# Performance work log

Measured on AMD Instinct MI355X. Metric: run time of the kernel, lower is better.

## Reference

```python
import jax, jax.numpy as jnp
import numpy as np

N = 50000        # nodes
E = 800000       # edges (before self-loops)
F_IN = 256       # input feature dim
HID = 64         # hidden per head (concat=False -> head mean)
NCLS = 40        # classes
HEADS = 8
NEG_SLOPE = 0.2  # PyG GATConv default leaky_relu slope


def setup_inputs() -> dict:
    key = jax.random.key(0)
    ks = jax.random.split(key, 11)
    s = 0.1
    return {
        "x": jax.random.normal(ks[0], (N, F_IN), jnp.float32),
        "edge_index": jax.random.randint(ks[1], (2, E), 0, N, dtype=jnp.int64),
        "edge_attr": jax.random.uniform(ks[2], (E, 1), jnp.float32),
        "W0": jax.random.normal(ks[3], (HEADS * HID, F_IN), jnp.float32) * s,
        "a0s": jax.random.normal(ks[4], (HEADS, HID), jnp.float32) * s,
        "a0d": jax.random.normal(ks[5], (HEADS, HID), jnp.float32) * s,
        "b0": jnp.zeros((HID,), jnp.float32),
        "W2": jax.random.normal(ks[6], (HEADS * NCLS, HID), jnp.float32) * s,
        "a2s": jax.random.normal(ks[7], (HEADS, NCLS), jnp.float32) * s,
        "a2d": jax.random.normal(ks[8], (HEADS, NCLS), jnp.float32) * s,
        "b2": jnp.zeros((NCLS,), jnp.float32),
    }


def _gat_conv(x, src, dst, W, att_src, att_dst, bias, heads, out_c):
    # Linear: [N, in] @ [heads*out, in]^T -> [N, heads, out]
    h = (x @ W.T).reshape(N, heads, out_c)
    # Per-node attention logits, gathered per edge.
    a_s = jnp.einsum('nhc,hc->nh', h, att_src)
    a_d = jnp.einsum('nhc,hc->nh', h, att_dst)
    e = jax.nn.leaky_relu(a_s[src] + a_d[dst], NEG_SLOPE)  # [E, H]
    # Segment softmax over incoming edges of each destination node.
    m = jax.ops.segment_max(e, dst, num_segments=N)
    p = jnp.exp(e - m[dst])
    denom = jax.ops.segment_sum(p, dst, num_segments=N)
    alpha = p / (denom[dst] + 1e-16)
    # Weighted message scatter-sum: [E,H,C] -> [N,H,C]
    out = jax.ops.segment_sum(alpha[:, :, None] * h[src], dst, num_segments=N)
    # concat=False -> mean over heads, then bias.
    return out.mean(axis=1) + bias


def reference(x, edge_index, edge_attr, W0, a0s, a0d, b0, W2, a2s, a2d, b2):
    # edge_attr is unpacked by the torch forward but never used by GATConv.
    # PyG GATConv adds self-loops by default.
    loops = jnp.arange(N, dtype=edge_index.dtype)
    src = jnp.concatenate([edge_index[0], loops])
    dst = jnp.concatenate([edge_index[1], loops])
    h = jax.nn.relu(_gat_conv(x, src, dst, W0, a0s, a0d, b0, HEADS, HID))
    # dropout is identity in eval mode
    out = _gat_conv(h, src, dst, W2, a2s, a2d, b2, HEADS, NCLS)
    return jax.nn.log_softmax(out, axis=1)
```

## Files before the change

### kernel.cpp

```cpp
#include <hip/hip_runtime.h>
#include <hip/hip_bf16.h>
#include <math.h>


#define NEG_SLOPE 0.2f

typedef short v8s __attribute__((ext_vector_type(8)));
typedef float v4f __attribute__((ext_vector_type(4)));
typedef float v2f __attribute__((ext_vector_type(2)));
typedef unsigned short u16;
typedef unsigned int u32;
typedef unsigned char u8;

__device__ __forceinline__ u16 f2bf(float f) {
    union { float f; u32 u; } v; v.f = f;
    u32 r = v.u + 0x7fffu + ((v.u >> 16) & 1u);
    return (u16)(r >> 16);
}
__device__ __forceinline__ float lrelu_exp(float e) {
    e = (e > 0.f) ? e : NEG_SLOPE * e;
    return __expf(e);
}
__device__ __forceinline__ void dec8(uint2 r, float* h) {
    v2f a = __builtin_amdgcn_cvt_pk_f32_fp8(r.x, false);
    v2f b = __builtin_amdgcn_cvt_pk_f32_fp8(r.x, true);
    v2f c = __builtin_amdgcn_cvt_pk_f32_fp8(r.y, false);
    v2f d = __builtin_amdgcn_cvt_pk_f32_fp8(r.y, true);
    h[0] = a.x; h[1] = a.y; h[2] = b.x; h[3] = b.y;
    h[4] = c.x; h[5] = c.y; h[6] = d.x; h[7] = d.y;
}
__device__ __forceinline__ u8 enc8(float v) {
    u32 p = __builtin_amdgcn_cvt_pk_fp8_f32(v, v, 0u, false);
    return (u8)(p & 0xffu);
}


__global__ __launch_bounds__(256) void hist_k(const int* __restrict__ ei, int* __restrict__ deg,
                                              int E, int Nn) {
    int e = blockIdx.x * 256 + threadIdx.x;
    int ET = E + Nn;
    if (e >= ET) return;
    int d = (e < E) ? ei[E + e] : (e - E);
    atomicAdd(&deg[d], 1);
}

__global__ __launch_bounds__(1024) void scanA_k(const int* __restrict__ deg, int* __restrict__ incl,
                                                int* __restrict__ bsum, int n) {
    __shared__ int wsum[16];
    int t = threadIdx.x;
    int i = blockIdx.x * 1024 + t;
    int v = (i < n) ? deg[i] : 0;
    int lane = t & 63, wid = t >> 6;
    int sv = v;
    for (int off = 1; off < 64; off <<= 1) {
        int u = __shfl_up(sv, off, 64);
        if (lane >= off) sv += u;
    }
    if (lane == 63) wsum[wid] = sv;
    __syncthreads();
    if (t < 16) {
        int w = wsum[t];
        for (int off = 1; off < 16; off <<= 1) {
            int u = __shfl_up(w, off, 64);
            if (t >= off) w += u;
        }
        wsum[t] = w;
    }
    __syncthreads();
    int pre = (wid > 0) ? wsum[wid - 1] : 0;
    int inc = pre + sv;
    if (i < n) incl[i] = inc;
    if (t == 1023) bsum[blockIdx.x] = inc;
}

__global__ __launch_bounds__(64) void scanB_k(const int* __restrict__ bsum, int* __restrict__ boff, int B) {
    int t = threadIdx.x;
    int v = (t < B) ? bsum[t] : 0;
    int sv = v;
    for (int off = 1; off < 64; off <<= 1) {
        int u = __shfl_up(sv, off, 64);
        if (t >= off) sv += u;
    }
    if (t < B) boff[t] = sv - v;
    if (t == 63) boff[B] = sv;
}

__global__ __launch_bounds__(256) void scanC_k(const int* __restrict__ incl, const int* __restrict__ deg,
                                               const int* __restrict__ boff, int* __restrict__ rowstart,
                                               int n, int B) {
    int i = blockIdx.x * 256 + threadIdx.x;
    if (i < n) rowstart[i] = boff[i >> 10] + incl[i] - deg[i];
    if (i == 0) rowstart[n] = boff[B];
}

__global__ __launch_bounds__(256) void scatter_k(const int* __restrict__ ei,
                                                 const int* __restrict__ rowstart,
                                                 int* __restrict__ cursor,
                                                 int* __restrict__ srcs, int E, int Nn) {
    int e = blockIdx.x * 256 + threadIdx.x;
    int ET = E + Nn;
    if (e >= ET) return;
    int s, d;
    if (e < E) { s = ei[e]; d = ei[E + e]; }
    else       { s = e - E; d = e - E; }
    int pos = atomicAdd(&cursor[d], 1);
    srcs[rowstart[d] + pos] = s;
}


__global__ __launch_bounds__(256) void cast3_k(const float* __restrict__ x, u16* __restrict__ xb, int nx,
                                               const float* __restrict__ W0, u16* __restrict__ W0b, int n0,
                                               const float* __restrict__ W2, u16* __restrict__ W2b, int n2) {
    int i = (blockIdx.x * 256 + threadIdx.x) * 4;
    const float* in; u16* out;
    if (i < nx)            { in = x;  out = xb; }
    else if (i < nx + n0)  { in = W0; out = W0b; i -= nx; }
    else if (i < nx + n0 + n2) { in = W2; out = W2b; i -= nx + n0; }
    else return;
    float4 v = *reinterpret_cast<const float4*>(in + i);
    ushort4 o;
    o.x = f2bf(v.x); o.y = f2bf(v.y); o.z = f2bf(v.z); o.w = f2bf(v.w);
    *reinterpret_cast<ushort4*>(out + i) = o;
}


__global__ __launch_bounds__(256, 4) void gemm_mfma(const u16* __restrict__ Ab,
                                                    const u16* __restrict__ Bb,
                                                    u8* __restrict__ Cf, int M, int Nc, int K,
                                                    const float* __restrict__ avs_vec,
                                                    const float* __restrict__ avd_vec,
                                                    float* as_out, float* ad_out) {
    __shared__ __align__(16) u8 lds[27648];
    u16 (*As)[72] = reinterpret_cast<u16(*)[72]>(lds);
    u16 (*Bs)[72] = reinterpret_cast<u16(*)[72]>(lds + 18432);
    const int t = threadIdx.x;
    const int m0 = blockIdx.x * 128;
    const int n0 = blockIdx.y * 64;
    const int w = t >> 6, lane = t & 63;
    const int wr = w * 32;
    const int q = lane >> 4, l16 = lane & 15;

    v4f acc[2][4];
#pragma unroll
    for (int i = 0; i < 2; i++)
#pragma unroll
        for (int j = 0; j < 4; j++) acc[i][j] = (v4f){0.f, 0.f, 0.f, 0.f};

    for (int kt = 0; kt < K; kt += 64) {
#pragma unroll
        for (int it = 0; it < 4; it++) {
            int c = it * 256 + t;
            int row = c >> 3, col8 = (c & 7) * 8;
            int gm = m0 + row;
            uint4 va = make_uint4(0u, 0u, 0u, 0u);
            if (gm < M) va = *reinterpret_cast<const uint4*>(Ab + (size_t)gm * K + kt + col8);
            *reinterpret_cast<uint4*>(&As[row][col8]) = va;
        }
#pragma unroll
        for (int it = 0; it < 2; it++) {
            int c = it * 256 + t;
            int row = c >> 3, col8 = (c & 7) * 8;
            uint4 vb = *reinterpret_cast<const uint4*>(Bb + (size_t)(n0 + row) * K + kt + col8);
            *reinterpret_cast<uint4*>(&Bs[row][col8]) = vb;
        }
        __syncthreads();
#pragma unroll
        for (int ks = 0; ks < 2; ks++) {
            v8s af[2], bf[4];
#pragma unroll
            for (int i = 0; i < 2; i++)
                af[i] = *reinterpret_cast<const v8s*>(&As[wr + i * 16 + l16][ks * 32 + q * 8]);
#pragma unroll
            for (int j = 0; j < 4; j++)
                bf[j] = *reinterpret_cast<const v8s*>(&Bs[j * 16 + l16][ks * 32 + q * 8]);
#pragma unroll
            for (int i = 0; i < 2; i++)
#pragma unroll
                for (int j = 0; j < 4; j++)
                    acc[i][j] = __builtin_amdgcn_mfma_f32_16x16x32_bf16(af[i], bf[j], acc[i][j], 0, 0, 0);
        }
        __syncthreads();
    }

    const bool do_att = (as_out != nullptr);
    float avs[4], avd[4];
    if (do_att) {
#pragma unroll
        for (int j = 0; j < 4; j++) {
            avs[j] = avs_vec[n0 + j * 16 + l16];
            avd[j] = avd_vec[n0 + j * 16 + l16];
        }
    }
    const int head = n0 >> 6;

    u8* Cs = lds;
#pragma unroll
    for (int i = 0; i < 2; i++) {
#pragma unroll
        for (int r = 0; r < 4; r++) {
            int row = wr + i * 16 + q * 4 + r;
#pragma unroll
            for (int j = 0; j < 4; j++)
                Cs[row * 80 + j * 16 + l16] = enc8(acc[i][j][r]);
            if (do_att) {
                int gm = m0 + row;
                float ps = 0.f, pd = 0.f;
#pragma unroll
                for (int j = 0; j < 4; j++) {
                    float v = acc[i][j][r];
                    ps = fmaf(v, avs[j], ps);
                    pd = fmaf(v, avd[j], pd);
                }
#pragma unroll
                for (int m = 1; m < 16; m <<= 1) {
                    ps += __shfl_xor(ps, m, 64);
                    pd += __shfl_xor(pd, m, 64);
                }
                if (l16 == 0 && gm < M) {
                    as_out[gm * 8 + head] = ps;
                    ad_out[gm * 8 + head] = pd;
                }
            }
        }
    }
    __syncthreads();
#pragma unroll
    for (int it = 0; it < 2; it++) {
        int idx = it * 256 + t;
        int row = idx >> 2, ch = idx & 3;
        int gm = m0 + row;
        if (gm < M)
            *reinterpret_cast<uint4*>(Cf + (size_t)gm * Nc + n0 + ch * 16) =
                *reinterpret_cast<const uint4*>(&Cs[row * 80 + ch * 16]);
    }
}


__global__ __launch_bounds__(256) void agg1_k(const u8* __restrict__ h1f,
                                              const float* __restrict__ as1, const float* __restrict__ ad1,
                                              const int* __restrict__ srcs, const int* __restrict__ rowstart,
                                              const float* __restrict__ b0, u16* __restrict__ x1b, int Nn) {
    int wave = threadIdx.x >> 6, lane = threadIdx.x & 63;
    int n = blockIdx.x * 4 + wave;
    if (n >= Nn) return;
    const int hl = lane >> 3;
    const float adl = ad1[n * 8 + hl];
    const u32 loff = (u32)lane * 8u;
    float acc[8] = {0, 0, 0, 0, 0, 0, 0, 0};
    float dsum = 0.f;
    int beg = rowstart[n], end = rowstart[n + 1];
    int i = beg;
    for (; i + 8 <= end; i += 8) {
        int s[8];
#pragma unroll
        for (int u = 0; u < 8; u++) s[u] = __builtin_amdgcn_readfirstlane(srcs[i + u]);
        uint2 rw[8];
#pragma unroll
        for (int u = 0; u < 8; u++) rw[u] = *reinterpret_cast<const uint2*>(h1f + ((u32)s[u] * 512u + loff));
        float eg[8];
#pragma unroll
        for (int u = 0; u < 8; u++) eg[u] = as1[(u32)s[u] * 8u + hl];
        float p[8];
#pragma unroll
        for (int u = 0; u < 8; u++) { p[u] = lrelu_exp(eg[u] + adl); dsum += p[u]; }
#pragma unroll
        for (int u = 0; u < 8; u++) {
            float hv[8];
            dec8(rw[u], hv);
#pragma unroll
            for (int j = 0; j < 8; j++) acc[j] = fmaf(p[u], hv[j], acc[j]);
        }
    }
    for (; i < end; i++) {
        int s = __builtin_amdgcn_readfirstlane(srcs[i]);
        uint2 raw = *reinterpret_cast<const uint2*>(h1f + ((u32)s * 512u + loff));
        float p = lrelu_exp(as1[(u32)s * 8u + hl] + adl);
        dsum += p;
        float hv[8];
        dec8(raw, hv);
#pragma unroll
        for (int j = 0; j < 8; j++) acc[j] = fmaf(p, hv[j], acc[j]);
    }
    float inv = 1.f / (dsum + 1e-16f);
    float r[8];
#pragma unroll
    for (int j = 0; j < 8; j++) r[j] = acc[j] * inv;
#pragma unroll
    for (int j = 0; j < 8; j++) {
        r[j] += __shfl_xor(r[j], 8, 64);
        r[j] += __shfl_xor(r[j], 16, 64);
        r[j] += __shfl_xor(r[j], 32, 64);
    }
    if (lane < 8) {
        u16 o[8];
#pragma unroll
        for (int j = 0; j < 8; j++) {
            float v = r[j] * 0.125f + b0[lane * 8 + j];
            o[j] = f2bf((v > 0.f) ? v : 0.f);
        }
        *reinterpret_cast<uint4*>(x1b + (size_t)n * 64 + lane * 8) =
            *reinterpret_cast<const uint4*>(o);
    }
}


__global__ __launch_bounds__(256) void att2_k(const u8* __restrict__ h2f,
                                              const float* __restrict__ a2s, const float* __restrict__ a2d,
                                              float* __restrict__ as2, float* __restrict__ ad2, int Nn) {
    int t = blockIdx.x * 256 + threadIdx.x;
    if (t >= Nn * 8) return;
    int n = t >> 3, h = t & 7;
    const u8* hr = h2f + (size_t)n * 320 + h * 40;
    float s1 = 0.f, s2 = 0.f;
#pragma unroll
    for (int b = 0; b < 5; b++) {
        uint2 raw = *reinterpret_cast<const uint2*>(hr + b * 8);
        float h8[8];
        dec8(raw, h8);
#pragma unroll
        for (int j = 0; j < 8; j++) {
            int c = h * 40 + b * 8 + j;
            s1 = fmaf(h8[j], a2s[c], s1);
            s2 = fmaf(h8[j], a2d[c], s2);
        }
    }
    as2[t] = s1;
    ad2[t] = s2;
}


__global__ __launch_bounds__(256) void agg2_k(const u8* __restrict__ h2f,
                                              const float* __restrict__ as2, const float* __restrict__ ad2,
                                              const int* __restrict__ srcs, const int* __restrict__ rowstart,
                                              const float* __restrict__ b2, float* __restrict__ out, int Nn) {
    __shared__ float smem[4][320];
    int wave = threadIdx.x >> 6, lane = threadIdx.x & 63;
    int n = blockIdx.x * 4 + wave;
    bool active = (n < Nn);
    bool ld = active && (lane < 40);
    const int hl = lane / 5;
    float adl = ld ? ad2[n * 8 + hl] : 0.f;
    float acc[8] = {0, 0, 0, 0, 0, 0, 0, 0};
    float dsum = 0.f;
    if (ld) {
        const u32 loff = (u32)lane * 8u;
        int beg = rowstart[n], end = rowstart[n + 1];
        int i = beg;
        for (; i + 8 <= end; i += 8) {
            int s[8];
#pragma unroll
            for (int u = 0; u < 8; u++) s[u] = __builtin_amdgcn_readfirstlane(srcs[i + u]);
            uint2 rw[8];
#pragma unroll
            for (int u = 0; u < 8; u++) rw[u] = *reinterpret_cast<const uint2*>(h2f + ((u32)s[u] * 320u + loff));
            float eg[8];
#pragma unroll
            for (int u = 0; u < 8; u++) eg[u] = as2[(u32)s[u] * 8u + hl];
            float p[8];
#pragma unroll
            for (int u = 0; u < 8; u++) { p[u] = lrelu_exp(eg[u] + adl); dsum += p[u]; }
#pragma unroll
            for (int u = 0; u < 8; u++) {
                float hv[8];
                dec8(rw[u], hv);
#pragma unroll
                for (int j = 0; j < 8; j++) acc[j] = fmaf(p[u], hv[j], acc[j]);
            }
        }
        for (; i < end; i++) {
            int s = __builtin_amdgcn_readfirstlane(srcs[i]);
            uint2 raw = *reinterpret_cast<const uint2*>(h2f + ((u32)s * 320u + loff));
            float p = lrelu_exp(as2[(u32)s * 8u + hl] + adl);
            dsum += p;
            float hv[8];
            dec8(raw, hv);
#pragma unroll
            for (int j = 0; j < 8; j++) acc[j] = fmaf(p, hv[j], acc[j]);
        }
        float inv = 1.f / (dsum + 1e-16f);
#pragma unroll
        for (int j = 0; j < 8; j++) smem[wave][lane * 8 + j] = acc[j] * inv;
    }
    __syncthreads();
    if (active) {
        float v;
        if (lane < 40) {
            float ssum = 0.f;
#pragma unroll
            for (int h = 0; h < 8; h++) ssum += smem[wave][h * 40 + lane];
            v = ssum * 0.125f + b2[lane];
        } else {
            v = -INFINITY;
        }
        float m = v;
        for (int off = 32; off > 0; off >>= 1) m = fmaxf(m, __shfl_xor(m, off, 64));
        float ex = (lane < 40) ? __expf(v - m) : 0.f;
        float se = ex;
        for (int off = 32; off > 0; off >>= 1) se += __shfl_xor(se, off, 64);
        if (lane < 40) out[(size_t)n * 40 + lane] = v - m - __logf(se);
    }
}


extern "C" void kernel_launch(void* const* d_in, const int* in_sizes, int n_in,
                              void* d_out, int out_size, void* d_ws, size_t ws_size,
                              hipStream_t stream) {
    const float* x   = (const float*)d_in[0];
    const int*   ei  = (const int*)d_in[1];
    const float* W0  = (const float*)d_in[3];
    const float* a0s = (const float*)d_in[4];
    const float* a0d = (const float*)d_in[5];
    const float* b0  = (const float*)d_in[6];
    const float* W2  = (const float*)d_in[7];
    const float* a2s = (const float*)d_in[8];
    const float* a2d = (const float*)d_in[9];
    const float* b2  = (const float*)d_in[10];
    float* out = (float*)d_out;

    const int Nn = in_sizes[0] / 256;
    const int E  = in_sizes[1] / 2;
    const int ET = E + Nn;
    const int NB = (Nn + 1023) / 1024;

    size_t off = 0;
    auto carve = [&](size_t bytes) -> void* {
        void* p = (char*)d_ws + off;
        off += (bytes + 255) & ~(size_t)255;
        return p;
    };
    u16*   xb       = (u16*)carve((size_t)Nn * 256 * 2);
    u16*   W0b      = (u16*)carve((size_t)512 * 256 * 2);
    u16*   W2b      = (u16*)carve((size_t)320 * 64 * 2);
    u8*    h1f      = (u8*)carve((size_t)Nn * 512);
    u16*   x1b      = (u16*)carve((size_t)Nn * 64 * 2);
    u8*    h2f      = (u8*)carve((size_t)Nn * 320);
    float* as1      = (float*)carve((size_t)Nn * 8 * 4);
    float* ad1      = (float*)carve((size_t)Nn * 8 * 4);
    float* as2      = (float*)carve((size_t)Nn * 8 * 4);
    float* ad2      = (float*)carve((size_t)Nn * 8 * 4);
    int*   deg      = (int*)carve((size_t)Nn * 4);
    int*   cursor   = (int*)carve((size_t)Nn * 4);
    int*   rowstart = (int*)carve((size_t)(Nn + 1) * 4);
    int*   srcs     = (int*)carve((size_t)ET * 4);
    int*   incl     = (int*)carve((size_t)Nn * 4);
    int*   bsum     = (int*)carve(64 * 4);
    int*   boff     = (int*)carve(65 * 4);

    const size_t degPad = ((size_t)Nn * 4 + 255) & ~(size_t)255;
    hipMemsetAsync(deg, 0, degPad + (size_t)Nn * 4, stream);

    hist_k<<<(ET + 255) / 256, 256, 0, stream>>>(ei, deg, E, Nn);
    scanA_k<<<NB, 1024, 0, stream>>>(deg, incl, bsum, Nn);
    scanB_k<<<1, 64, 0, stream>>>(bsum, boff, NB);
    scanC_k<<<(Nn + 255) / 256, 256, 0, stream>>>(incl, deg, boff, rowstart, Nn, NB);
    scatter_k<<<(ET + 255) / 256, 256, 0, stream>>>(ei, rowstart, cursor, srcs, E, Nn);

    const int nx = Nn * 256, n0c = 512 * 256, n2c = 320 * 64;
    cast3_k<<<((nx + n0c + n2c) / 4 + 255) / 256, 256, 0, stream>>>(
        x, xb, nx, W0, W0b, n0c, W2, W2b, n2c);

    gemm_mfma<<<dim3((Nn + 127) / 128, 8), 256, 0, stream>>>(
        xb, W0b, h1f, Nn, 512, 256, a0s, a0d, as1, ad1);
    agg1_k<<<(Nn + 3) / 4, 256, 0, stream>>>(h1f, as1, ad1, srcs, rowstart, b0, x1b, Nn);

    gemm_mfma<<<dim3((Nn + 127) / 128, 5), 256, 0, stream>>>(
        x1b, W2b, h2f, Nn, 320, 64, nullptr, nullptr, nullptr, nullptr);
    att2_k<<<(Nn * 8 + 255) / 256, 256, 0, stream>>>(h2f, a2s, a2d, as2, ad2, Nn);
    agg2_k<<<(Nn + 3) / 4, 256, 0, stream>>>(h2f, as2, ad2, srcs, rowstart, b2, out, Nn);
}
```

Before: 399.6 us.

## Fuse CSR build and bf16 casts into one cooperative persistent kernel

Replaces the memset, histogram, three scan kernels, scatter, and cast kernel with a single cooperative kernel using grid-wide syncs between phases. It is meant to remove several kernel launch gaps and the separate memset. The cast work is folded into the first phase alongside the zeroing. The risk is that grid.sync barriers and a fixed grid of 256 blocks of 1024 threads may underuse the GPU for the bandwidth-heavy cast and scatter phases.

```diff
diff --git a/kernel.cpp b/kernel.cpp
--- a/kernel.cpp
+++ b/kernel.cpp
@@ -1,9 +1,12 @@
 #include <hip/hip_runtime.h>
 #include <hip/hip_bf16.h>
+#include <hip/hip_cooperative_groups.h>
 #include <math.h>
 
 
 #define NEG_SLOPE 0.2f
+
+namespace cg = cooperative_groups;
 
 typedef short v8s __attribute__((ext_vector_type(8)));
 typedef float v4f __attribute__((ext_vector_type(4)));
@@ -35,92 +38,93 @@
 }
 
 
-__global__ __launch_bounds__(256) void hist_k(const int* __restrict__ ei, int* __restrict__ deg,
-                                              int E, int Nn) {
-    int e = blockIdx.x * 256 + threadIdx.x;
-    int ET = E + Nn;
-    if (e >= ET) return;
-    int d = (e < E) ? ei[E + e] : (e - E);
-    atomicAdd(&deg[d], 1);
-}
-
-__global__ __launch_bounds__(1024) void scanA_k(const int* __restrict__ deg, int* __restrict__ incl,
-                                                int* __restrict__ bsum, int n) {
+__global__ __launch_bounds__(1024) void prep_k(const float* __restrict__ x, u16* __restrict__ xb,
+                                               const float* __restrict__ W0, u16* __restrict__ W0b,
+                                               const float* __restrict__ W2, u16* __restrict__ W2b,
+                                               int nx, int n0c, int n2c,
+                                               const int* __restrict__ ei, int* __restrict__ deg,
+                                               int* __restrict__ cursor, int* __restrict__ incl,
+                                               int* __restrict__ bsum, int* __restrict__ rowstart,
+                                               int* __restrict__ srcs, int E, int Nn, int NB) {
+    cg::grid_group grid = cg::this_grid();
     __shared__ int wsum[16];
-    int t = threadIdx.x;
-    int i = blockIdx.x * 1024 + t;
-    int v = (i < n) ? deg[i] : 0;
-    int lane = t & 63, wid = t >> 6;
-    int sv = v;
-    for (int off = 1; off < 64; off <<= 1) {
-        int u = __shfl_up(sv, off, 64);
-        if (lane >= off) sv += u;
-    }
-    if (lane == 63) wsum[wid] = sv;
+    __shared__ int sb[65];
+    const int T = gridDim.x * blockDim.x;
+    const int tid = blockIdx.x * blockDim.x + threadIdx.x;
+    const int ET = E + Nn;
+
+    for (int i = tid; i < Nn; i += T) { deg[i] = 0; cursor[i] = 0; }
+    const int tot4 = (nx + n0c + n2c) >> 2;
+    for (int i4 = tid; i4 < tot4; i4 += T) {
+        int i = i4 << 2;
+        const float* in; u16* out;
+        if (i < nx)            { in = x;  out = xb; }
+        else if (i < nx + n0c) { in = W0; out = W0b; i -= nx; }
+        else                   { in = W2; out = W2b; i -= nx + n0c; }
+        float4 v = *reinterpret_cast<const float4*>(in + i);
+        ushort4 o;
+        o.x = f2bf(v.x); o.y = f2bf(v.y); o.z = f2bf(v.z); o.w = f2bf(v.w);
+        *reinterpret_cast<ushort4*>(out + i) = o;
+    }
+    grid.sync();
+
+    for (int e = tid; e < ET; e += T) {
+        int d = (e < E) ? ei[E + e] : (e - E);
+        atomicAdd(&deg[d], 1);
+    }
+    grid.sync();
+
+    if (blockIdx.x < NB) {
+        int t = threadIdx.x;
+        int i = blockIdx.x * 1024 + t;
+        int v = (i < Nn) ? deg[i] : 0;
+        int lane = t & 63, wid = t >> 6;
+        int sv = v;
+        for (int off = 1; off < 64; off <<= 1) {
+            int u = __shfl_up(sv, off, 64);
+            if (lane >= off) sv += u;
+        }
+        if (lane == 63) wsum[wid] = sv;
+        __syncthreads();
+        if (t < 16) {
+            int w = wsum[t];
+            for (int off = 1; off < 16; off <<= 1) {
+                int u = __shfl_up(w, off, 64);
+                if (t >= off) w += u;
+            }
+            wsum[t] = w;
+        }
+        __syncthreads();
+        int pre = (wid > 0) ? wsum[wid - 1] : 0;
+        int inc = pre + sv;
+        if (i < Nn) incl[i] = inc;
+        if (t == 1023) bsum[blockIdx.x] = inc;
+    }
+    grid.sync();
+
+    if (threadIdx.x < 64) {
+        int t = threadIdx.x;
+        int v = (t < NB) ? bsum[t] : 0;
+        int sv = v;
+        for (int off = 1; off < 64; off <<= 1) {
+            int u = __shfl_up(sv, off, 64);
+            if (t >= off) sv += u;
+        }
+        sb[t] = sv - v;
+        if (t == 63) sb[64] = sv;
+    }
     __syncthreads();
-    if (t < 16) {
-        int w = wsum[t];
-        for (int off = 1; off < 16; off <<= 1) {
-            int u = __shfl_up(w, off, 64);
-            if (t >= off) w += u;
-        }
-        wsum[t] = w;
-    }
-    __syncthreads();
-    int pre = (wid > 0) ? wsum[wid - 1] : 0;
-    int inc = pre + sv;
-    if (i < n) incl[i] = inc;
-    if (t == 1023) bsum[blockIdx.x] = inc;
-}
-
-__global__ __launch_bounds__(64) void scanB_k(const int* __restrict__ bsum, int* __restrict__ boff, int B) {
-    int t = threadIdx.x;
-    int v = (t < B) ? bsum[t] : 0;
-    int sv = v;
-    for (int off = 1; off < 64; off <<= 1) {
-        int u = __shfl_up(sv, off, 64);
-        if (t >= off) sv += u;
-    }
-    if (t < B) boff[t] = sv - v;
-    if (t == 63) boff[B] = sv;
-}
-
-__global__ __launch_bounds__(256) void scanC_k(const int* __restrict__ incl, const int* __restrict__ deg,
-                                               const int* __restrict__ boff, int* __restrict__ rowstart,
-                                               int n, int B) {
-    int i = blockIdx.x * 256 + threadIdx.x;
-    if (i < n) rowstart[i] = boff[i >> 10] + incl[i] - deg[i];
-    if (i == 0) rowstart[n] = boff[B];
-}
-
-__global__ __launch_bounds__(256) void scatter_k(const int* __restrict__ ei,
-                                                 const int* __restrict__ rowstart,
-                                                 int* __restrict__ cursor,
-                                                 int* __restrict__ srcs, int E, int Nn) {
-    int e = blockIdx.x * 256 + threadIdx.x;
-    int ET = E + Nn;
-    if (e >= ET) return;
-    int s, d;
-    if (e < E) { s = ei[e]; d = ei[E + e]; }
-    else       { s = e - E; d = e - E; }
-    int pos = atomicAdd(&cursor[d], 1);
-    srcs[rowstart[d] + pos] = s;
-}
-
-
-__global__ __launch_bounds__(256) void cast3_k(const float* __restrict__ x, u16* __restrict__ xb, int nx,
-                                               const float* __restrict__ W0, u16* __restrict__ W0b, int n0,
-                                               const float* __restrict__ W2, u16* __restrict__ W2b, int n2) {
-    int i = (blockIdx.x * 256 + threadIdx.x) * 4;
-    const float* in; u16* out;
-    if (i < nx)            { in = x;  out = xb; }
-    else if (i < nx + n0)  { in = W0; out = W0b; i -= nx; }
-    else if (i < nx + n0 + n2) { in = W2; out = W2b; i -= nx + n0; }
-    else return;
-    float4 v = *reinterpret_cast<const float4*>(in + i);
-    ushort4 o;
-    o.x = f2bf(v.x); o.y = f2bf(v.y); o.z = f2bf(v.z); o.w = f2bf(v.w);
-    *reinterpret_cast<ushort4*>(out + i) = o;
+    for (int i = tid; i < Nn; i += T) rowstart[i] = sb[i >> 10] + incl[i] - deg[i];
+    if (tid == 0) rowstart[Nn] = sb[64];
+    grid.sync();
+
+    for (int e = tid; e < ET; e += T) {
+        int s, d;
+        if (e < E) { s = ei[e]; d = ei[E + e]; }
+        else       { s = e - E; d = e - E; }
+        int pos = atomicAdd(&cursor[d], 1);
+        srcs[rowstart[d] + pos] = s;
+    }
 }
 
 
@@ -417,10 +421,10 @@
     const float* b2  = (const float*)d_in[10];
     float* out = (float*)d_out;
 
-    const int Nn = in_sizes[0] / 256;
-    const int E  = in_sizes[1] / 2;
+    int Nn = in_sizes[0] / 256;
+    int E  = in_sizes[1] / 2;
     const int ET = E + Nn;
-    const int NB = (Nn + 1023) / 1024;
+    int NB = (Nn + 1023) / 1024;
 
     size_t off = 0;
     auto carve = [&](size_t bytes) -> void* {
@@ -444,20 +448,16 @@
     int*   srcs     = (int*)carve((size_t)ET * 4);
     int*   incl     = (int*)carve((size_t)Nn * 4);
     int*   bsum     = (int*)carve(64 * 4);
-    int*   boff     = (int*)carve(65 * 4);
-
-    const size_t degPad = ((size_t)Nn * 4 + 255) & ~(size_t)255;
-    hipMemsetAsync(deg, 0, degPad + (size_t)Nn * 4, stream);
-
-    hist_k<<<(ET + 255) / 256, 256, 0, stream>>>(ei, deg, E, Nn);
-    scanA_k<<<NB, 1024, 0, stream>>>(deg, incl, bsum, Nn);
-    scanB_k<<<1, 64, 0, stream>>>(bsum, boff, NB);
-    scanC_k<<<(Nn + 255) / 256, 256, 0, stream>>>(incl, deg, boff, rowstart, Nn, NB);
-    scatter_k<<<(ET + 255) / 256, 256, 0, stream>>>(ei, rowstart, cursor, srcs, E, Nn);
-
-    const int nx = Nn * 256, n0c = 512 * 256, n2c = 320 * 64;
-    cast3_k<<<((nx + n0c + n2c) / 4 + 255) / 256, 256, 0, stream>>>(
-        x, xb, nx, W0, W0b, n0c, W2, W2b, n2c);
+
+    int nx = Nn * 256, n0c = 512 * 256, n2c = 320 * 64;
+
+    void* args[] = {
+        (void*)&x, (void*)&xb, (void*)&W0, (void*)&W0b, (void*)&W2, (void*)&W2b,
+        (void*)&nx, (void*)&n0c, (void*)&n2c,
+        (void*)&ei, (void*)&deg, (void*)&cursor, (void*)&incl, (void*)&bsum,
+        (void*)&rowstart, (void*)&srcs, (void*)&E, (void*)&Nn, (void*)&NB
+    };
+    hipLaunchCooperativeKernel((const void*)prep_k, dim3(256), dim3(1024), args, 0, stream);
 
     gemm_mfma<<<dim3((Nn + 127) / 128, 8), 256, 0, stream>>>(
         xb, W0b, h1f, Nn, 512, 256, a0s, a0d, as1, ad1);
```

Result: slower. 538.8 us (+34.8%).
